# Optimization experiments

Measured on AMD Instinct MI355X. Metric: run time of the kernel, lower is better.

The kernel has to match this reference:

```python
import jax, jax.numpy as jnp
import numpy as np

B, D, H = 64, 512, 512          # batch c, spatial dim D, feature dim H == channel
CIN = 4 * H                     # concat of 4 branches
HID = CIN // 4                  # reduction=4


def _gcn_norm_adj():
    # fixed 4-node fully-connected graph, GCNConv default: add self loops,
    # symmetric normalization D^{-1/2} (A+I) D^{-1/2}
    ei = np.array([[0, 1, 0, 2, 0, 3, 1, 2, 1, 3, 2, 3],
                   [1, 0, 2, 0, 3, 0, 2, 1, 3, 1, 3, 2]])
    A = np.zeros((4, 4), np.float32)
    A[ei[1], ei[0]] = 1.0               # message src -> dst
    A += np.eye(4, dtype=np.float32)    # self loops
    dinv = 1.0 / np.sqrt(A.sum(1))
    return jnp.asarray(dinv[:, None] * A * dinv[None, :])  # (4,4)


def setup_inputs() -> dict:
    key = jax.random.key(0)
    ks = jax.random.split(key, 32)

    def rn(k, shape, s=0.02):
        return jax.random.normal(k, shape, dtype=jnp.float32) * s

    inp = {}
    for i in range(4):
        inp[f"fea{i+1}"] = jax.random.normal(ks[i], (B, D, H), dtype=jnp.float32)
    inp["W_gcn"] = rn(ks[4], (H, H))
    inp["b_gcn"] = jnp.zeros((H,), jnp.float32)
    for i in range(4):
        inp[f"W1_{i+1}"] = rn(ks[5 + 4 * i], (CIN, HID))
        inp[f"b1_{i+1}"] = jnp.zeros((HID,), jnp.float32)
        inp[f"W2_{i+1}"] = rn(ks[6 + 4 * i], (HID, H))
        inp[f"b2_{i+1}"] = jnp.zeros((H,), jnp.float32)
    return inp


def reference(fea1, fea2, fea3, fea4, W_gcn, b_gcn,
              W1_1, b1_1, W2_1, b2_1,
              W1_2, b1_2, W2_2, b2_2,
              W1_3, b1_3, W2_3, b2_3,
              W1_4, b1_4, W2_4, b2_4):
    A = _gcn_norm_adj()                                   # (4,4)
    y = jnp.stack((fea1, fea2, fea3, fea4), axis=1)       # (B,4,D,H)
    # GCNConv batched over all samples: Ahat_norm @ (X W) + b
    xw = jnp.einsum('bndh,hk->bndk', y, W_gcn)            # (B,4,D,H)
    yg = jnp.einsum('mn,bndk->bmdk', A, xw) + b_gcn       # (B,4,D,H)
    z = jnp.concatenate([yg[:, 0], yg[:, 1], yg[:, 2], yg[:, 3]], axis=2)  # (B,D,4H)

    def gate(W1, b1, W2, b2, fea):
        h = jax.nn.relu(z @ W1 + b1)                      # (B,D,HID)
        g = jax.nn.sigmoid(h @ W2 + b2)                   # (B,D,H)
        return jax.nn.relu(g) * fea

    return (gate(W1_1, b1_1, W2_1, b2_1, fea1),
            gate(W1_2, b1_2, W2_2, b2_2, fea2),
            gate(W1_3, b1_3, W2_3, b2_3, fea3),
            gate(W1_4, b1_4, W2_4, b2_4, fea4))
```

## Files before the change

### kernel.cpp

```cpp
#include <hip/hip_runtime.h>
#include <math.h>

#define MM 32768
#define KK 512
#define NN 512
#define BM 128
#define BN 128
#define BK 32

typedef float  f32x4  __attribute__((ext_vector_type(4)));
typedef __bf16 bf16x8 __attribute__((ext_vector_type(8)));
typedef unsigned short u16x8 __attribute__((ext_vector_type(8)));

__device__ __forceinline__ unsigned short f2bf(float f) {
    union { float f; unsigned int u; } v; v.f = f;
    unsigned int r = v.u + 0x7fffu + ((v.u >> 16) & 1u);
    return (unsigned short)(r >> 16);
}

__device__ __forceinline__ void gl_lds16(const void* g, void* l) {
    __builtin_amdgcn_global_load_lds((const __attribute__((address_space(1))) void*)g,
                                     (__attribute__((address_space(3))) void*)l,
                                     16, 0, 0);
}

__global__ __launch_bounds__(256)
void fsum_cast(const float* __restrict__ f1, const float* __restrict__ f2,
               const float* __restrict__ f3, const float* __restrict__ f4,
               unsigned short* __restrict__ out)
{
    const long i = ((long)blockIdx.x * 256 + threadIdx.x) * 8;
    f32x4 s0 = *(const f32x4*)(f1 + i);
    f32x4 s1 = *(const f32x4*)(f1 + i + 4);
    s0 += *(const f32x4*)(f2 + i);  s1 += *(const f32x4*)(f2 + i + 4);
    s0 += *(const f32x4*)(f3 + i);  s1 += *(const f32x4*)(f3 + i + 4);
    s0 += *(const f32x4*)(f4 + i);  s1 += *(const f32x4*)(f4 + i + 4);
    u16x8 o;
    o[0] = f2bf(s0[0]); o[1] = f2bf(s0[1]); o[2] = f2bf(s0[2]); o[3] = f2bf(s0[3]);
    o[4] = f2bf(s1[0]); o[5] = f2bf(s1[1]); o[6] = f2bf(s1[2]); o[7] = f2bf(s1[3]);
    *(u16x8*)(out + i) = o;
}

struct WArgs {
    const float* src[9];
    unsigned short* dst[9];
};

__global__ __launch_bounds__(256)
void wprep(WArgs a)
{
    __shared__ float t[32][33];
    const int z  = blockIdx.z;
    const float* __restrict__ src = a.src[z];
    unsigned short* __restrict__ dst = a.dst[z];
    const int k0 = blockIdx.x * 32;
    const int n0 = blockIdx.y * 32;
    const int tx = threadIdx.x;
    for (int kk = threadIdx.y; kk < 32; kk += 8) {
        float v = src[(long)(k0 + kk) * 512 + n0 + tx];
        if (z >= 1 && z <= 4) {
            v += src[(long)(512  + k0 + kk) * 512 + n0 + tx];
            v += src[(long)(1024 + k0 + kk) * 512 + n0 + tx];
            v += src[(long)(1536 + k0 + kk) * 512 + n0 + tx];
        }
        if (z == 0) v *= 0.25f;
        t[kk][tx] = v;
    }
    __syncthreads();
    for (int nn = threadIdx.y; nn < 32; nn += 8) {
        dst[(long)(n0 + nn) * 512 + k0 + tx] = f2bf(t[tx][nn]);
    }
}

template<int MODE>
__global__ __launch_bounds__(256)
void gemm_ep(const unsigned short* __restrict__ A,
             const unsigned short* __restrict__ Bt,
             const float* __restrict__ bias,
             const float* __restrict__ fea,
             void* __restrict__ out)
{
    __shared__ unsigned short As[BM * BK];
    __shared__ unsigned short Bs[BN * BK];

    const int tid  = threadIdx.x;
    const int lane = tid & 63;
    const int wave = tid >> 6;
    const int m0 = blockIdx.x * BM;
    const int n0 = blockIdx.y * BN;

    const bool isA = (wave < 2);
    const int rowbase = (wave & 1) * 64;
    const unsigned short* gsrc = isA ? A : Bt;
    unsigned short* ldst = isA ? As : Bs;
    const int r  = lane >> 2;
    const int cb = lane & 3;
    const long grow0 = (isA ? (long)m0 : (long)n0) + rowbase;
    const unsigned short* gbase0 = gsrc + grow0 * KK + cb * 8;
    unsigned short* lbase = ldst + rowbase * BK;

    const int frow = lane & 15;
    const int fk   = (lane >> 4) * 8;
    const int wrow = wave >> 1;
    const int wcol = wave & 1;

    f32x4 acc[4][4] = {};

    for (int ks = 0; ks < KK / BK; ++ks) {
        const unsigned short* gb = gbase0 + ks * BK;
        #pragma unroll
        for (int c = 0; c < 4; ++c) {
            gl_lds16(gb + (long)(c * 16 + r) * KK, lbase + c * 16 * BK);
        }
        __syncthreads();

        bf16x8 afr[4], bfr[4];
        #pragma unroll
        for (int i = 0; i < 4; ++i)
            afr[i] = *(const bf16x8*)(As + (wrow * 64 + i * 16 + frow) * BK + fk);
        #pragma unroll
        for (int j = 0; j < 4; ++j)
            bfr[j] = *(const bf16x8*)(Bs + (wcol * 64 + j * 16 + frow) * BK + fk);

        #pragma unroll
        for (int i = 0; i < 4; ++i)
            #pragma unroll
            for (int j = 0; j < 4; ++j)
                acc[i][j] = __builtin_amdgcn_mfma_f32_16x16x32_bf16(
                    afr[i], bfr[j], acc[i][j], 0, 0, 0);
        __syncthreads();
    }

    const int cq = (lane >> 4) * 4;
    const int cc = lane & 15;
    #pragma unroll
    for (int j = 0; j < 4; ++j) {
        const int col = n0 + wcol * 64 + j * 16 + cc;
        const float bv = bias[col];
        #pragma unroll
        for (int i = 0; i < 4; ++i) {
            #pragma unroll
            for (int rr = 0; rr < 4; ++rr) {
                const int row = m0 + wrow * 64 + i * 16 + cq + rr;
                float v = acc[i][j][rr] + bv;
                if (MODE == 0) {
                    ((unsigned short*)out)[(long)row * NN + col] = f2bf(v);
                } else if (MODE == 1) {
                    ((unsigned short*)out)[(long)row * NN + col] = f2bf(fmaxf(v, 0.0f));
                } else {
                    const float g = 1.0f / (1.0f + __expf(-v));
                    ((float*)out)[(long)row * NN + col] =
                        g * fea[(long)row * NN + col];
                }
            }
        }
    }
}

extern "C" void kernel_launch(void* const* d_in, const int* in_sizes, int n_in,
                              void* d_out, int out_size, void* d_ws, size_t ws_size,
                              hipStream_t stream)
{
    (void)in_sizes; (void)n_in; (void)out_size; (void)ws_size;

    const float* fea[4] = {(const float*)d_in[0], (const float*)d_in[1],
                           (const float*)d_in[2], (const float*)d_in[3]};
    const float* W_gcn = (const float*)d_in[4];
    const float* b_gcn = (const float*)d_in[5];
    const float *W1[4], *b1[4], *W2[4], *b2[4];
    for (int i = 0; i < 4; ++i) {
        W1[i] = (const float*)d_in[6 + 4 * i];
        b1[i] = (const float*)d_in[7 + 4 * i];
        W2[i] = (const float*)d_in[8 + 4 * i];
        b2[i] = (const float*)d_in[9 + 4 * i];
    }

    char* ws = (char*)d_ws;
    unsigned short* fsum_h = (unsigned short*)ws;
    unsigned short* s_buf  = (unsigned short*)(ws + (size_t)33554432);
    unsigned short* wbuf   = (unsigned short*)(ws + (size_t)67108864);
    unsigned short* WgT = wbuf;
    unsigned short *W1T[4], *W2T[4];
    for (int i = 0; i < 4; ++i) {
        W1T[i] = wbuf + (size_t)(1 + i) * 262144;
        W2T[i] = wbuf + (size_t)(5 + i) * 262144;
    }

    fsum_cast<<<8192, 256, 0, stream>>>(fea[0], fea[1], fea[2], fea[3], fsum_h);

    WArgs wa;
    wa.src[0] = W_gcn; wa.dst[0] = WgT;
    for (int i = 0; i < 4; ++i) { wa.src[1 + i] = W1[i]; wa.dst[1 + i] = W1T[i]; }
    for (int i = 0; i < 4; ++i) { wa.src[5 + i] = W2[i]; wa.dst[5 + i] = W2T[i]; }
    wprep<<<dim3(16, 16, 9), dim3(32, 8), 0, stream>>>(wa);

    const dim3 ggrid(MM / BM, NN / BN);
    gemm_ep<0><<<ggrid, 256, 0, stream>>>(fsum_h, WgT, b_gcn, nullptr, s_buf);

    float* outp = (float*)d_out;
    for (int i = 0; i < 4; ++i) {
        gemm_ep<1><<<ggrid, 256, 0, stream>>>(s_buf, W1T[i], b1[i], nullptr, fsum_h);
        gemm_ep<2><<<ggrid, 256, 0, stream>>>(fsum_h, W2T[i], b2[i], fea[i],
                                              outp + (size_t)i * MM * NN);
    }
}
```

Baseline: 857.7 us.

## Fold GCN weight into W1, batch branches in one grid, double-buffer GEMM

Precomputes Wc = Wg·W1sum per branch with a small GEMM, and folds b_gcn through W1 into a combined bias. This removes the large 32768x512 GCN GEMM and its intermediate buffer. The gate GEMMs for all four branches now run as single launches over a z-dimension, the K loop uses double-buffered LDS prefetch, and the epilogue is reorganised (swapped MFMA operands) so each lane stores four contiguous columns as a vector. Rounding Wc to bf16 changes numerics slightly, and the per-branch hidden buffers raise workspace use.

```diff
diff --git a/kernel.cpp b/kernel.cpp
--- a/kernel.cpp
+++ b/kernel.cpp
@@ -11,11 +11,17 @@
 typedef float  f32x4  __attribute__((ext_vector_type(4)));
 typedef __bf16 bf16x8 __attribute__((ext_vector_type(8)));
 typedef unsigned short u16x8 __attribute__((ext_vector_type(8)));
+typedef unsigned short u16x4 __attribute__((ext_vector_type(4)));
 
 __device__ __forceinline__ unsigned short f2bf(float f) {
     union { float f; unsigned int u; } v; v.f = f;
     unsigned int r = v.u + 0x7fffu + ((v.u >> 16) & 1u);
     return (unsigned short)(r >> 16);
+}
+
+__device__ __forceinline__ float bf2f(unsigned short h) {
+    union { unsigned int u; float f; } v; v.u = ((unsigned int)h) << 16;
+    return v.f;
 }
 
 __device__ __forceinline__ void gl_lds16(const void* g, void* l) {
@@ -56,6 +62,13 @@
     const int k0 = blockIdx.x * 32;
     const int n0 = blockIdx.y * 32;
     const int tx = threadIdx.x;
+    if (z == 0) {
+        for (int kk = threadIdx.y; kk < 32; kk += 8) {
+            float v = src[(long)(k0 + kk) * 512 + n0 + tx];
+            dst[(long)(k0 + kk) * 512 + n0 + tx] = f2bf(0.25f * v);
+        }
+        return;
+    }
     for (int kk = threadIdx.y; kk < 32; kk += 8) {
         float v = src[(long)(k0 + kk) * 512 + n0 + tx];
         if (z >= 1 && z <= 4) {
@@ -63,7 +76,6 @@
             v += src[(long)(1024 + k0 + kk) * 512 + n0 + tx];
             v += src[(long)(1536 + k0 + kk) * 512 + n0 + tx];
         }
-        if (z == 0) v *= 0.25f;
         t[kk][tx] = v;
     }
     __syncthreads();
@@ -72,16 +84,62 @@
     }
 }
 
+struct BArgs {
+    const unsigned short* w1t[4];
+    const float* b1[4];
+    float* out[4];
+};
+
+__global__ __launch_bounds__(256)
+void bprep(const float* __restrict__ bg, BArgs a)
+{
+    __shared__ float bgs[512];
+    const int z = blockIdx.x;
+    const int tid = threadIdx.x;
+    bgs[tid]       = bg[tid];
+    bgs[tid + 256] = bg[tid + 256];
+    __syncthreads();
+    const unsigned short* __restrict__ w = a.w1t[z];
+    for (int n = tid; n < 512; n += 256) {
+        float acc = 0.0f;
+        const unsigned short* row = w + (long)n * 512;
+        #pragma unroll 4
+        for (int t = 0; t < 512; t += 8) {
+            u16x8 wv = *(const u16x8*)(row + t);
+            #pragma unroll
+            for (int jj = 0; jj < 8; ++jj) acc += bgs[t + jj] * bf2f(wv[jj]);
+        }
+        a.out[z][n] = acc + a.b1[z][n];
+    }
+}
+
+struct GArgs {
+    const unsigned short* A[4];
+    const unsigned short* Bt[4];
+    const float* bias[4];
+    const float* fea[4];
+    void* out[4];
+};
+
+__device__ __forceinline__ void stage4(const unsigned short* gb, unsigned short* lb, int r) {
+    #pragma unroll
+    for (int c = 0; c < 4; ++c)
+        gl_lds16(gb + (long)(c * 16 + r) * KK, lb + c * 16 * BK);
+}
+
 template<int MODE>
 __global__ __launch_bounds__(256)
-void gemm_ep(const unsigned short* __restrict__ A,
-             const unsigned short* __restrict__ Bt,
-             const float* __restrict__ bias,
-             const float* __restrict__ fea,
-             void* __restrict__ out)
-{
-    __shared__ unsigned short As[BM * BK];
-    __shared__ unsigned short Bs[BN * BK];
+void gemm_ep(GArgs a)
+{
+    __shared__ unsigned short As[2][BM * BK];
+    __shared__ unsigned short Bs[2][BN * BK];
+
+    const int z = blockIdx.z;
+    const unsigned short* __restrict__ A  = a.A[z];
+    const unsigned short* __restrict__ Bt = a.Bt[z];
+    const float* __restrict__ bias = a.bias[z];
+    const float* __restrict__ fea  = a.fea[z];
+    void* __restrict__ out = a.out[z];
 
     const int tid  = threadIdx.x;
     const int lane = tid & 63;
@@ -92,12 +150,12 @@
     const bool isA = (wave < 2);
     const int rowbase = (wave & 1) * 64;
     const unsigned short* gsrc = isA ? A : Bt;
-    unsigned short* ldst = isA ? As : Bs;
     const int r  = lane >> 2;
     const int cb = lane & 3;
     const long grow0 = (isA ? (long)m0 : (long)n0) + rowbase;
     const unsigned short* gbase0 = gsrc + grow0 * KK + cb * 8;
-    unsigned short* lbase = ldst + rowbase * BK;
+    unsigned short* lb0 = (isA ? As[0] : Bs[0]) + rowbase * BK;
+    unsigned short* lb1 = (isA ? As[1] : Bs[1]) + rowbase * BK;
 
     const int frow = lane & 15;
     const int fk   = (lane >> 4) * 8;
@@ -106,52 +164,66 @@
 
     f32x4 acc[4][4] = {};
 
+    stage4(gbase0, lb0, r);
+    __syncthreads();
+
+    #pragma unroll 2
     for (int ks = 0; ks < KK / BK; ++ks) {
-        const unsigned short* gb = gbase0 + ks * BK;
-        #pragma unroll
-        for (int c = 0; c < 4; ++c) {
-            gl_lds16(gb + (long)(c * 16 + r) * KK, lbase + c * 16 * BK);
-        }
-        __syncthreads();
-
+        const bool odd = (ks & 1);
+        if (ks + 1 < KK / BK)
+            stage4(gbase0 + (ks + 1) * BK, odd ? lb0 : lb1, r);
+
+        const unsigned short* Asc = odd ? As[1] : As[0];
+        const unsigned short* Bsc = odd ? Bs[1] : Bs[0];
         bf16x8 afr[4], bfr[4];
         #pragma unroll
         for (int i = 0; i < 4; ++i)
-            afr[i] = *(const bf16x8*)(As + (wrow * 64 + i * 16 + frow) * BK + fk);
+            afr[i] = *(const bf16x8*)(Asc + (wrow * 64 + i * 16 + frow) * BK + fk);
         #pragma unroll
         for (int j = 0; j < 4; ++j)
-            bfr[j] = *(const bf16x8*)(Bs + (wcol * 64 + j * 16 + frow) * BK + fk);
+            bfr[j] = *(const bf16x8*)(Bsc + (wcol * 64 + j * 16 + frow) * BK + fk);
 
         #pragma unroll
         for (int i = 0; i < 4; ++i)
             #pragma unroll
             for (int j = 0; j < 4; ++j)
                 acc[i][j] = __builtin_amdgcn_mfma_f32_16x16x32_bf16(
-                    afr[i], bfr[j], acc[i][j], 0, 0, 0);
+                    bfr[j], afr[i], acc[i][j], 0, 0, 0);
+
         __syncthreads();
     }
 
-    const int cq = (lane >> 4) * 4;
-    const int cc = lane & 15;
+    const int mr  = lane & 15;
+    const int cq4 = (lane >> 4) * 4;
     #pragma unroll
     for (int j = 0; j < 4; ++j) {
-        const int col = n0 + wcol * 64 + j * 16 + cc;
-        const float bv = bias[col];
+        const int col = n0 + wcol * 64 + j * 16 + cq4;
+        f32x4 bv;
+        if (MODE == 3) { bv[0] = bv[1] = bv[2] = bv[3] = 0.0f; }
+        else           { bv = *(const f32x4*)(bias + col); }
         #pragma unroll
         for (int i = 0; i < 4; ++i) {
-            #pragma unroll
-            for (int rr = 0; rr < 4; ++rr) {
-                const int row = m0 + wrow * 64 + i * 16 + cq + rr;
-                float v = acc[i][j][rr] + bv;
-                if (MODE == 0) {
-                    ((unsigned short*)out)[(long)row * NN + col] = f2bf(v);
-                } else if (MODE == 1) {
-                    ((unsigned short*)out)[(long)row * NN + col] = f2bf(fmaxf(v, 0.0f));
-                } else {
-                    const float g = 1.0f / (1.0f + __expf(-v));
-                    ((float*)out)[(long)row * NN + col] =
-                        g * fea[(long)row * NN + col];
+            const long row = m0 + wrow * 64 + i * 16 + mr;
+            f32x4 v = acc[i][j] + bv;
+            if (MODE == 1) {
+                u16x4 o;
+                o[0] = f2bf(fmaxf(v[0], 0.0f)); o[1] = f2bf(fmaxf(v[1], 0.0f));
+                o[2] = f2bf(fmaxf(v[2], 0.0f)); o[3] = f2bf(fmaxf(v[3], 0.0f));
+                *(u16x4*)((unsigned short*)out + row * NN + col) = o;
+            } else if (MODE == 3) {
+                u16x4 o;
+                o[0] = f2bf(v[0]); o[1] = f2bf(v[1]);
+                o[2] = f2bf(v[2]); o[3] = f2bf(v[3]);
+                *(u16x4*)((unsigned short*)out + row * NN + col) = o;
+            } else {
+                f32x4 fv = *(const f32x4*)(fea + row * NN + col);
+                f32x4 o;
+                #pragma unroll
+                for (int q = 0; q < 4; ++q) {
+                    float e = __expf(-v[q]);
+                    o[q] = __fdividef(fv[q], 1.0f + e);
                 }
+                *(f32x4*)((float*)out + row * NN + col) = o;
             }
         }
     }
@@ -175,32 +247,51 @@
         b2[i] = (const float*)d_in[9 + 4 * i];
     }
 
+    const size_t MB = 1024 * 1024;
     char* ws = (char*)d_ws;
     unsigned short* fsum_h = (unsigned short*)ws;
-    unsigned short* s_buf  = (unsigned short*)(ws + (size_t)33554432);
-    unsigned short* wbuf   = (unsigned short*)(ws + (size_t)67108864);
-    unsigned short* WgT = wbuf;
-    unsigned short *W1T[4], *W2T[4];
+    unsigned short* wbuf   = (unsigned short*)(ws + 32 * MB);
+    unsigned short* Wgb = wbuf;
+    unsigned short *W1T[4], *W2T[4], *WcT[4], *hbuf[4];
     for (int i = 0; i < 4; ++i) {
         W1T[i] = wbuf + (size_t)(1 + i) * 262144;
         W2T[i] = wbuf + (size_t)(5 + i) * 262144;
-    }
+        WcT[i] = (unsigned short*)(ws + 40 * MB) + (size_t)i * 262144;
+        hbuf[i] = (unsigned short*)(ws + 48 * MB + (size_t)i * 32 * MB);
+    }
+    float* bcomb = (float*)(ws + 44 * MB);
 
     fsum_cast<<<8192, 256, 0, stream>>>(fea[0], fea[1], fea[2], fea[3], fsum_h);
 
     WArgs wa;
-    wa.src[0] = W_gcn; wa.dst[0] = WgT;
+    wa.src[0] = W_gcn; wa.dst[0] = Wgb;
     for (int i = 0; i < 4; ++i) { wa.src[1 + i] = W1[i]; wa.dst[1 + i] = W1T[i]; }
     for (int i = 0; i < 4; ++i) { wa.src[5 + i] = W2[i]; wa.dst[5 + i] = W2T[i]; }
     wprep<<<dim3(16, 16, 9), dim3(32, 8), 0, stream>>>(wa);
 
-    const dim3 ggrid(MM / BM, NN / BN);
-    gemm_ep<0><<<ggrid, 256, 0, stream>>>(fsum_h, WgT, b_gcn, nullptr, s_buf);
+    BArgs ba;
+    for (int i = 0; i < 4; ++i) { ba.w1t[i] = W1T[i]; ba.b1[i] = b1[i]; ba.out[i] = bcomb + (size_t)i * 512; }
+    bprep<<<4, 256, 0, stream>>>(b_gcn, ba);
+
+    GArgs g3;
+    for (int i = 0; i < 4; ++i) {
+        g3.A[i] = W1T[i]; g3.Bt[i] = Wgb; g3.bias[i] = nullptr;
+        g3.fea[i] = nullptr; g3.out[i] = WcT[i];
+    }
+    gemm_ep<3><<<dim3(4, 4, 4), 256, 0, stream>>>(g3);
+
+    GArgs g1;
+    for (int i = 0; i < 4; ++i) {
+        g1.A[i] = fsum_h; g1.Bt[i] = WcT[i]; g1.bias[i] = bcomb + (size_t)i * 512;
+        g1.fea[i] = nullptr; g1.out[i] = hbuf[i];
+    }
+    gemm_ep<1><<<dim3(MM / BM, NN / BN, 4), 256, 0, stream>>>(g1);
 
     float* outp = (float*)d_out;
-    for (int i = 0; i < 4; ++i) {
-        gemm_ep<1><<<ggrid, 256, 0, stream>>>(s_buf, W1T[i], b1[i], nullptr, fsum_h);
-        gemm_ep<2><<<ggrid, 256, 0, stream>>>(fsum_h, W2T[i], b2[i], fea[i],
-                                              outp + (size_t)i * MM * NN);
-    }
-}
+    GArgs g2;
+    for (int i = 0; i < 4; ++i) {
+        g2.A[i] = hbuf[i]; g2.Bt[i] = W2T[i]; g2.bias[i] = b2[i];
+        g2.fea[i] = fea[i]; g2.out[i] = outp + (size_t)i * MM * NN;
+    }
+    gemm_ep<2><<<dim3(MM / BM, NN / BN, 4), 256, 0, stream>>>(g2);
+}
```

Measured after the change: 838.6 us. 2.2% less time.
